# Kernel tuning notes

Hardware: AMD Instinct MI355X
Metric: run time of the kernel (lower is better)

## Reference

```python
import jax, jax.numpy as jnp
import numpy as np

THRESH = 0.7
MIN_KEPT = 10000
ALPHA = 0.25
GAMMA = 2.0

B, C, H, W = 8, 8, 1024, 1024


def setup_inputs() -> dict:
    key = jax.random.key(0)
    k1, k2 = jax.random.split(key)
    inp = jax.random.normal(k1, (B, C, H, W), dtype=jnp.float32)
    tgt = jax.random.randint(k2, (B, C, H, W), 0, 2, dtype=jnp.int32)
    return {"input": inp, "target": tgt}


def _focal_mean(logits, targets, kept):
    # binary_cross_entropy_with_logits, elementwise, numerically stable
    bce = jnp.maximum(logits, 0.0) - logits * targets + jnp.log1p(jnp.exp(-jnp.abs(logits)))
    pt = jnp.exp(-bce)
    fl = ALPHA * (1.0 - pt) ** GAMMA * bce
    kf = kept.astype(fl.dtype)
    # mean over kept (gathered) elements == masked sum / count
    return jnp.sum(fl * kf) / jnp.maximum(jnp.sum(kf), 1.0)


def _channel0_loss(input, target):
    # NOTE: the torch source slices [:, [0, i]] but then always reads index 0,
    # i.e. every loop iteration operates on original channel 0.
    logits0 = input[:, 0]                              # [B, H, W]
    ygt = target[:, 0].astype(jnp.float32)             # [B, H, W]
    probs = jax.nn.sigmoid(logits0)
    # OHEM keep mask: positives with prob <= thresh, negatives with prob >= 1-thresh
    kept = jnp.where(ygt == 1.0, probs <= THRESH,
                     jnp.where(ygt == 0.0, probs >= 1.0 - THRESH, False))
    # fallback: if too few kept, force-keep the min_kept hardest (closest to 0.5)
    hardness = jnp.abs(probs - 0.5).reshape(-1)
    _, idx = jax.lax.top_k(-hardness, MIN_KEPT)
    topk_mask = jnp.zeros(hardness.shape, bool).at[idx].set(True).reshape(kept.shape)
    kept = jnp.where(jnp.sum(kept) < MIN_KEPT, kept | topk_mask, kept)
    return _focal_mean(logits0, ygt, kept)


def reference(input, target):
    n_cls = input.shape[1]
    # loop over i in 1..C-1 computes the identical channel-0 loss each time
    return jnp.asarray(n_cls - 1, jnp.float32) * _channel0_loss(input, target)
```

## Files before the change

kernel.cpp:

```cpp
#include <hip/hip_runtime.h>
#include <hip/hip_bf16.h>


#define NBLK 1024
#define NTHR 256

__device__ __forceinline__ void fl_accum(float x, int y, float& s, int& c) {
    const float T = 0.8472978603872037f;
    float z    = y ? x : -x;
    bool  kept = (z <= T);
    float u    = __expf(-fabsf(z));
    float pm   = __builtin_amdgcn_rcpf(1.0f + u);
    float pt   = (z >= 0.0f) ? pm : u * pm;
    float bce  = -__logf(pt);
    float om   = 1.0f - pt;
    float fl   = 0.25f * om * om * bce;
    s += kept ? fl : 0.0f;
    c += kept ? 1 : 0;
}

__global__ __launch_bounds__(NTHR) void ohem_fl_partial(
    const float4* __restrict__ in4, const int4* __restrict__ tg4,
    double* __restrict__ psum, unsigned* __restrict__ pcnt) {
    const int tid = threadIdx.x;
    const int bid = blockIdx.x;
    const int b   = bid >> 7;
    const int off = ((bid & 127) << 11) + tid;
    const size_t base = ((size_t)b << 21) + (size_t)off;

    float4 x[8];
    int4   y[8];
#pragma unroll
    for (int k = 0; k < 8; ++k) {
        x[k] = in4[base + (size_t)(k << 8)];
        y[k] = tg4[base + (size_t)(k << 8)];
    }

    float s = 0.0f;
    int   c = 0;
#pragma unroll
    for (int k = 0; k < 8; ++k) {
        fl_accum(x[k].x, y[k].x, s, c);
        fl_accum(x[k].y, y[k].y, s, c);
        fl_accum(x[k].z, y[k].z, s, c);
        fl_accum(x[k].w, y[k].w, s, c);
    }

    double ds = (double)s;
#pragma unroll
    for (int st = 32; st > 0; st >>= 1) {
        ds += __shfl_down(ds, st, 64);
        c  += __shfl_down(c,  st, 64);
    }
    __shared__ double   ws_s[NTHR / 64];
    __shared__ int      ws_c[NTHR / 64];
    const int wave = tid >> 6;
    if ((tid & 63) == 0) { ws_s[wave] = ds; ws_c[wave] = c; }
    __syncthreads();
    if (tid == 0) {
        double ts = 0.0; int tc = 0;
#pragma unroll
        for (int w = 0; w < NTHR / 64; ++w) { ts += ws_s[w]; tc += ws_c[w]; }
        psum[bid] = ts;
        pcnt[bid] = (unsigned)tc;
    }
}

__global__ __launch_bounds__(NTHR) void ohem_fl_final(
    const double* __restrict__ psum, const unsigned* __restrict__ pcnt,
    float* __restrict__ out) {
    const int tid = threadIdx.x;
    double s = 0.0;
    unsigned long long c = 0ull;
#pragma unroll
    for (int i = 0; i < NBLK / NTHR; ++i) {
        s += psum[i * NTHR + tid];
        c += (unsigned long long)pcnt[i * NTHR + tid];
    }
#pragma unroll
    for (int st = 32; st > 0; st >>= 1) {
        s += __shfl_down(s, st, 64);
        c += __shfl_down(c, st, 64);
    }
    __shared__ double             ws_s[NTHR / 64];
    __shared__ unsigned long long ws_c[NTHR / 64];
    const int wave = tid >> 6;
    if ((tid & 63) == 0) { ws_s[wave] = s; ws_c[wave] = c; }
    __syncthreads();
    if (tid == 0) {
        double ts = 0.0; unsigned long long tc = 0ull;
#pragma unroll
        for (int w = 0; w < NTHR / 64; ++w) { ts += ws_s[w]; tc += ws_c[w]; }
        double denom = fmax((double)tc, 1.0);
        out[0] = 7.0f * (float)(ts / denom);
    }
}

extern "C" void kernel_launch(void* const* d_in, const int* in_sizes, int n_in,
                              void* d_out, int out_size, void* d_ws, size_t ws_size,
                              hipStream_t stream) {
    const float4* in4 = (const float4*)d_in[0];
    const int4*   tg4 = (const int4*)d_in[1];
    float*        out = (float*)d_out;

    double*   psum = (double*)d_ws;
    unsigned* pcnt = (unsigned*)((char*)d_ws + NBLK * sizeof(double));

    ohem_fl_partial<<<NBLK, NTHR, 0, stream>>>(in4, tg4, psum, pcnt);
    ohem_fl_final<<<1, NTHR, 0, stream>>>(psum, pcnt, out);
}
```

Measured before the change: 19.84 us.

## Fuse partial and final reductions into one cooperative kernel with grid sync

Replaces the two-kernel reduction with a single cooperative launch. Each of the now half as many blocks processes twice the data in two load batches, publishes its partials with atomics, and then passes a grid-wide barrier, after which block 0 does the final reduction. This removes the second kernel launch and its gap, at the cost of grid-sync overhead and the constraint that every block must be resident at once. Halving the block count also changes per-block work and occupancy.

```diff
diff --git a/kernel.cpp b/kernel.cpp
--- a/kernel.cpp
+++ b/kernel.cpp
@@ -1,8 +1,11 @@
 #include <hip/hip_runtime.h>
 #include <hip/hip_bf16.h>
+#include <hip/hip_cooperative_groups.h>
+
+namespace cg = cooperative_groups;
 
 
-#define NBLK 1024
+#define NBLK 512
 #define NTHR 256
 
 __device__ __forceinline__ void fl_accum(float x, int y, float& s, int& c) {
@@ -19,31 +22,36 @@
     c += kept ? 1 : 0;
 }
 
-__global__ __launch_bounds__(NTHR) void ohem_fl_partial(
+__global__ __launch_bounds__(NTHR, 2) void ohem_fl_coop(
     const float4* __restrict__ in4, const int4* __restrict__ tg4,
-    double* __restrict__ psum, unsigned* __restrict__ pcnt) {
+    unsigned long long* __restrict__ slot_sum,
+    unsigned long long* __restrict__ slot_cnt,
+    float* __restrict__ out) {
     const int tid = threadIdx.x;
     const int bid = blockIdx.x;
-    const int b   = bid >> 7;
-    const int off = ((bid & 127) << 11) + tid;
+    const int b   = bid >> 6;
+    const int off = ((bid & 63) << 12) + tid;
     const size_t base = ((size_t)b << 21) + (size_t)off;
-
-    float4 x[8];
-    int4   y[8];
-#pragma unroll
-    for (int k = 0; k < 8; ++k) {
-        x[k] = in4[base + (size_t)(k << 8)];
-        y[k] = tg4[base + (size_t)(k << 8)];
-    }
 
     float s = 0.0f;
     int   c = 0;
 #pragma unroll
-    for (int k = 0; k < 8; ++k) {
-        fl_accum(x[k].x, y[k].x, s, c);
-        fl_accum(x[k].y, y[k].y, s, c);
-        fl_accum(x[k].z, y[k].z, s, c);
-        fl_accum(x[k].w, y[k].w, s, c);
+    for (int half = 0; half < 2; ++half) {
+        float4 x[8];
+        int4   y[8];
+#pragma unroll
+        for (int k = 0; k < 8; ++k) {
+            size_t g = base + (size_t)(((half << 3) + k) << 8);
+            x[k] = in4[g];
+            y[k] = tg4[g];
+        }
+#pragma unroll
+        for (int k = 0; k < 8; ++k) {
+            fl_accum(x[k].x, y[k].x, s, c);
+            fl_accum(x[k].y, y[k].y, s, c);
+            fl_accum(x[k].z, y[k].z, s, c);
+            fl_accum(x[k].w, y[k].w, s, c);
+        }
     }
 
     double ds = (double)s;
@@ -52,8 +60,8 @@
         ds += __shfl_down(ds, st, 64);
         c  += __shfl_down(c,  st, 64);
     }
-    __shared__ double   ws_s[NTHR / 64];
-    __shared__ int      ws_c[NTHR / 64];
+    __shared__ double ws_s[NTHR / 64];
+    __shared__ int    ws_c[NTHR / 64];
     const int wave = tid >> 6;
     if ((tid & 63) == 0) { ws_s[wave] = ds; ws_c[wave] = c; }
     __syncthreads();
@@ -61,36 +69,36 @@
         double ts = 0.0; int tc = 0;
 #pragma unroll
         for (int w = 0; w < NTHR / 64; ++w) { ts += ws_s[w]; tc += ws_c[w]; }
-        psum[bid] = ts;
-        pcnt[bid] = (unsigned)tc;
+        atomicExch(&slot_sum[bid], (unsigned long long)__double_as_longlong(ts));
+        atomicExch(&slot_cnt[bid], (unsigned long long)tc);
     }
-}
 
-__global__ __launch_bounds__(NTHR) void ohem_fl_final(
-    const double* __restrict__ psum, const unsigned* __restrict__ pcnt,
-    float* __restrict__ out) {
-    const int tid = threadIdx.x;
-    double s = 0.0;
-    unsigned long long c = 0ull;
+    cg::this_grid().sync();
+
+    if (bid != 0) return;
+
+    double fs = 0.0;
+    unsigned long long fc = 0ull;
 #pragma unroll
     for (int i = 0; i < NBLK / NTHR; ++i) {
-        s += psum[i * NTHR + tid];
-        c += (unsigned long long)pcnt[i * NTHR + tid];
+        unsigned long long sb = atomicAdd(&slot_sum[i * NTHR + tid], 0ull);
+        unsigned long long cb = atomicAdd(&slot_cnt[i * NTHR + tid], 0ull);
+        fs += __longlong_as_double((long long)sb);
+        fc += cb;
     }
 #pragma unroll
     for (int st = 32; st > 0; st >>= 1) {
-        s += __shfl_down(s, st, 64);
-        c += __shfl_down(c, st, 64);
+        fs += __shfl_down(fs, st, 64);
+        fc += __shfl_down(fc, st, 64);
     }
-    __shared__ double             ws_s[NTHR / 64];
-    __shared__ unsigned long long ws_c[NTHR / 64];
-    const int wave = tid >> 6;
-    if ((tid & 63) == 0) { ws_s[wave] = s; ws_c[wave] = c; }
+    __shared__ double             fs_s[NTHR / 64];
+    __shared__ unsigned long long fs_c[NTHR / 64];
+    if ((tid & 63) == 0) { fs_s[wave] = fs; fs_c[wave] = fc; }
     __syncthreads();
     if (tid == 0) {
         double ts = 0.0; unsigned long long tc = 0ull;
 #pragma unroll
-        for (int w = 0; w < NTHR / 64; ++w) { ts += ws_s[w]; tc += ws_c[w]; }
+        for (int w = 0; w < NTHR / 64; ++w) { ts += fs_s[w]; tc += fs_c[w]; }
         double denom = fmax((double)tc, 1.0);
         out[0] = 7.0f * (float)(ts / denom);
     }
@@ -103,9 +111,11 @@
     const int4*   tg4 = (const int4*)d_in[1];
     float*        out = (float*)d_out;
 
-    double*   psum = (double*)d_ws;
-    unsigned* pcnt = (unsigned*)((char*)d_ws + NBLK * sizeof(double));
+    unsigned long long* slot_sum = (unsigned long long*)d_ws;
+    unsigned long long* slot_cnt = slot_sum + NBLK;
 
-    ohem_fl_partial<<<NBLK, NTHR, 0, stream>>>(in4, tg4, psum, pcnt);
-    ohem_fl_final<<<1, NTHR, 0, stream>>>(psum, pcnt, out);
+    void* args[] = {(void*)&in4, (void*)&tg4, (void*)&slot_sum,
+                    (void*)&slot_cnt, (void*)&out};
+    hipLaunchCooperativeKernel((const void*)ohem_fl_coop, dim3(NBLK), dim3(NTHR),
+                               args, 0, stream);
 }
```

After: 77.63 us. +291.2%, slower.
